# Kernel optimization log

Hardware: AMD Instinct MI355X
Metric: run time of the kernel (lower is better)

The kernel has to match this reference:

```python
import jax, jax.numpy as jnp
import numpy as np

N_NODES = 100000
FEAT = 256
HID = 128
REL = 2
BATCH = 20000
K = 10  # filtersize


def setup_inputs() -> dict:
    key = jax.random.key(0)
    k1, k2, k3, k4, k5 = jax.random.split(key, 5)
    nodes = jax.random.randint(k1, (BATCH,), 0, N_NODES)
    neigh_idx = jax.random.randint(k2, (REL, BATCH, K), 0, N_NODES)
    features = jax.random.normal(k3, (N_NODES, FEAT), dtype=jnp.float32)
    W_stc = jax.random.normal(k4, (REL, FEAT, HID), dtype=jnp.float32) * (1.0 / np.sqrt(FEAT))
    W_det = jax.random.normal(k5, (FEAT + REL * HID, HID), dtype=jnp.float32) * (1.0 / np.sqrt(FEAT + REL * HID))
    return {"nodes": nodes, "neigh_idx": neigh_idx, "features": features,
            "W_stc": W_stc, "W_det": W_det}


def reference(nodes, neigh_idx, features, W_stc, W_det):
    # self features: irregular gather [B, F]
    self_feats = features[nodes]
    # per-relation neighbor gather [R, B, K, F] -> mean over sampled neighbors [R, B, F]
    neigh_mean = features[neigh_idx].mean(axis=2)
    # STC layer projection to hidden per relation: [R, B, H]
    neigh_h = jnp.einsum('rbf,rfh->rbh', neigh_mean, W_stc)
    # concat self feats with each relation's neighbor embedding: [B, F + R*H]
    combined = jnp.concatenate(
        [self_feats, jnp.moveaxis(neigh_h, 0, 1).reshape(neigh_h.shape[1], -1)], axis=1)
    # linear + relu (dropout_flag=False -> no dropout)
    return jax.nn.relu(combined @ W_det)
```

## Files before the change

kernel.cpp:

```cpp
#include <hip/hip_runtime.h>
#include <hip/hip_bf16.h>

#define N_NODES 100000
#define FEAT    256
#define HID     128
#define REL     2
#define BATCH   20000
#define KNEI    10

#define APAD    8
#define AROW    (768 + APAD)

typedef short bf16x8 __attribute__((ext_vector_type(8)));
typedef float f32x4  __attribute__((ext_vector_type(4)));

__device__ __forceinline__ unsigned short f2bf(float x) {
    union { float f; unsigned u; } v; v.f = x;
    unsigned r = v.u + 0x7fffu + ((v.u >> 16) & 1u);
    return (unsigned short)(r >> 16);
}

__device__ __forceinline__ ushort4 pack4(float a, float b, float c, float d) {
    ushort4 p; p.x = f2bf(a); p.y = f2bf(b); p.z = f2bf(c); p.w = f2bf(d);
    return p;
}

__device__ __forceinline__ size_t bsw_index(int k, int n) {
    int kt = k >> 5, j = k & 7, hi = (k >> 3) & 3;
    int lane = hi * 16 + (n & 15), nt = n >> 4;
    return ((size_t)(kt * 8 + nt) * 64 + lane) * 8 + j;
}

__global__ __launch_bounds__(256) void prep_B(const float* __restrict__ W_stc,
                                              const float* __restrict__ W_det,
                                              unsigned short* __restrict__ Bsw) {
    const int blk = blockIdx.x;
    const int tid = threadIdx.x;
    if (blk < 256) {
        const int rel = blk >> 7;
        const int f   = (blk & 127) * 2 + (tid >> 7);
        const int n   = tid & 127;
        const float* ws = W_stc + (size_t)(rel * FEAT + f) * HID;
        const float* wd = W_det + (size_t)(256 + rel * HID) * HID + n;
        float acc = 0.f;
        #pragma unroll
        for (int j = 0; j < HID; ++j) acc += ws[j] * wd[(size_t)j * HID];
        Bsw[bsw_index(256 + rel * 256 + f, n)] = f2bf(acc);
    } else {
        const int base = (blk - 256) * 2048;
        #pragma unroll
        for (int i = 0; i < 8; ++i) {
            const int idx = base + i * 256 + tid;
            const int k = idx >> 7, n = idx & 127;
            Bsw[bsw_index(k, n)] = f2bf(W_det[idx]);
        }
    }
}

__global__ __launch_bounds__(256, 4) void fused(const int* __restrict__ nodes,
                                                const int* __restrict__ neigh_idx,
                                                const float* __restrict__ features,
                                                const unsigned short* __restrict__ Bsw,
                                                float* __restrict__ out) {
    __shared__ unsigned short As[16 * AROW];
    __shared__ int idxs[336];

    const int blk  = blockIdx.x;
    const int tid  = threadIdx.x;
    const int w    = tid >> 6;
    const int lane = tid & 63;
    const float inv = 1.0f / (float)KNEI;

    {
        if (tid < 16)       idxs[tid] = nodes[blk * 16 + tid];
        else if (tid < 176) idxs[tid] = neigh_idx[blk * 160 + (tid - 16)];
        else                idxs[tid] = neigh_idx[BATCH * KNEI + blk * 160 + (tid - 176)];
        const int t2 = tid + 256;
        if (t2 < 336)       idxs[t2] = neigh_idx[BATCH * KNEI + blk * 160 + (t2 - 176)];
    }
    __syncthreads();

    const unsigned lnoff = (unsigned)lane << 4;
    #pragma unroll
    for (int e = 0; e < 4; ++e) {
        const int m = w * 4 + e;

        int ia[11], ib[10];
        ia[0] = idxs[m];
        #pragma unroll
        for (int k = 0; k < KNEI; ++k) ia[1 + k] = idxs[16 + m * KNEI + k];
        #pragma unroll
        for (int k = 0; k < KNEI; ++k) ib[k]     = idxs[176 + m * KNEI + k];

        f32x4 ta[11];
        #pragma unroll
        for (int k = 0; k < 11; ++k) {
            const unsigned voff = ((unsigned)ia[k] << 10) + lnoff;
            asm volatile("global_load_dwordx4 %0, %1, %2"
                         : "=v"(ta[k]) : "v"(voff), "s"(features));
        }
        f32x4 tb[10];
        #pragma unroll
        for (int k = 0; k < KNEI; ++k) {
            const unsigned voff = ((unsigned)ib[k] << 10) + lnoff;
            asm volatile("global_load_dwordx4 %0, %1, %2"
                         : "=v"(tb[k]) : "v"(voff), "s"(features));
        }

        asm volatile("s_waitcnt vmcnt(10)" ::: "memory");
        __builtin_amdgcn_sched_barrier(0);

        f32x4 s0 = ta[1];
        #pragma unroll
        for (int k = 2; k < 11; ++k) s0 += ta[k];

        ushort4* row = (ushort4*)(As + m * AROW);
        row[lane]      = pack4(ta[0][0], ta[0][1], ta[0][2], ta[0][3]);
        row[64 + lane] = pack4(s0[0] * inv, s0[1] * inv, s0[2] * inv, s0[3] * inv);

        asm volatile("s_waitcnt vmcnt(0)" ::: "memory");
        __builtin_amdgcn_sched_barrier(0);

        f32x4 s1 = tb[0];
        #pragma unroll
        for (int k = 1; k < KNEI; ++k) s1 += tb[k];
        row[128 + lane] = pack4(s1[0] * inv, s1[1] * inv, s1[2] * inv, s1[3] * inv);
    }
    __syncthreads();

    const int quad = lane >> 4;
    const int l16  = lane & 15;
    const unsigned short* a_base = As + l16 * AROW + quad * 8;

    f32x4 acc0 = (f32x4){0.f, 0.f, 0.f, 0.f};
    f32x4 acc1 = (f32x4){0.f, 0.f, 0.f, 0.f};
    const int nt0 = w, nt1 = w + 4;

    #pragma unroll
    for (int kt = 0; kt < 24; ++kt) {
        bf16x8 a = *(const bf16x8*)(a_base + kt * 32);
        const unsigned short* bk = Bsw + ((size_t)(kt * 8) * 64 + lane) * 8;
        bf16x8 b0 = *(const bf16x8*)(bk + (size_t)nt0 * 64 * 8);
        bf16x8 b1 = *(const bf16x8*)(bk + (size_t)nt1 * 64 * 8);
        acc0 = __builtin_amdgcn_mfma_f32_16x16x32_bf16(a, b0, acc0, 0, 0, 0);
        acc1 = __builtin_amdgcn_mfma_f32_16x16x32_bf16(a, b1, acc1, 0, 0, 0);
    }

    float* orow = out + (size_t)(blk * 16) * HID;
    #pragma unroll
    for (int r = 0; r < 4; ++r) {
        const int row = quad * 4 + r;
        float v0 = acc0[r];
        float v1 = acc1[r];
        orow[(size_t)row * HID + nt0 * 16 + l16] = v0 > 0.f ? v0 : 0.f;
        orow[(size_t)row * HID + nt1 * 16 + l16] = v1 > 0.f ? v1 : 0.f;
    }
}

extern "C" void kernel_launch(void* const* d_in, const int* in_sizes, int n_in,
                              void* d_out, int out_size, void* d_ws, size_t ws_size,
                              hipStream_t stream) {
    const int*   nodes     = (const int*)d_in[0];
    const int*   neigh_idx = (const int*)d_in[1];
    const float* features  = (const float*)d_in[2];
    const float* W_stc     = (const float*)d_in[3];
    const float* W_det     = (const float*)d_in[4];
    float* out = (float*)d_out;

    unsigned short* Bsw = (unsigned short*)d_ws;

    prep_B<<<272, 256, 0, stream>>>(W_stc, W_det, Bsw);
    fused<<<BATCH / 16, 256, 0, stream>>>(nodes, neigh_idx, features, Bsw, out);
}
```

Baseline: 197.7 us.

## Pre-project all node features through W_stc, then gather projected rows

Adds a pass that multiplies every node's features by both relation W_stc matrices (fp16 MFMA) into a workspace table P. The fused kernel then averages gathered 128-wide fp16 rows of P instead of 256-wide fp32 feature rows, and its final GEMM shrinks from K=768 to K=512. Operands move from bf16 to fp16. The aim is to cut random-gather traffic, at the cost of a dense pass over all nodes (reading every feature row and writing P) and a large workspace requirement. The old path is kept as a fallback when the workspace is too small.

```diff
diff --git a/kernel.cpp b/kernel.cpp
--- a/kernel.cpp
+++ b/kernel.cpp
@@ -8,22 +8,194 @@
 #define BATCH   20000
 #define KNEI    10
 
-#define APAD    8
-#define AROW    (768 + APAD)
-
-typedef short bf16x8 __attribute__((ext_vector_type(8)));
-typedef float f32x4  __attribute__((ext_vector_type(4)));
+typedef short  bf16x8 __attribute__((ext_vector_type(8)));
+typedef _Float16 half8 __attribute__((ext_vector_type(8)));
+typedef float  f32x4  __attribute__((ext_vector_type(4)));
+
+__device__ __forceinline__ unsigned short f2h(float x) {
+    union { _Float16 h; unsigned short u; } t; t.h = (_Float16)x; return t.u;
+}
+__device__ __forceinline__ ushort4 pack4h(float a, float b, float c, float d) {
+    ushort4 p; p.x = f2h(a); p.y = f2h(b); p.z = f2h(c); p.w = f2h(d); return p;
+}
 
 __device__ __forceinline__ unsigned short f2bf(float x) {
     union { float f; unsigned u; } v; v.f = x;
     unsigned r = v.u + 0x7fffu + ((v.u >> 16) & 1u);
     return (unsigned short)(r >> 16);
 }
-
 __device__ __forceinline__ ushort4 pack4(float a, float b, float c, float d) {
-    ushort4 p; p.x = f2bf(a); p.y = f2bf(b); p.z = f2bf(c); p.w = f2bf(d);
-    return p;
-}
+    ushort4 p; p.x = f2bf(a); p.y = f2bf(b); p.z = f2bf(c); p.w = f2bf(d); return p;
+}
+
+__device__ __forceinline__ size_t bswi(int k, int n, int NT) {
+    int kt = k >> 5, j = k & 7, hi = (k >> 3) & 3;
+    int lane = hi * 16 + (n & 15), nt = n >> 4;
+    return ((size_t)(kt * NT + nt) * 64 + lane) * 8 + j;
+}
+
+
+__global__ __launch_bounds__(256) void prep_Bf16(const float* __restrict__ W_stc,
+                                                 const float* __restrict__ W_det,
+                                                 unsigned short* __restrict__ Bsw_det,
+                                                 unsigned short* __restrict__ Bsw_stc) {
+    const int blk = blockIdx.x, tid = threadIdx.x;
+    if (blk < 64) {
+        #pragma unroll
+        for (int i = 0; i < 4; ++i) {
+            const int idx = blk * 1024 + i * 256 + tid;
+            const int k = idx >> 7, n = idx & 127;
+            Bsw_det[bswi(k, n, 8)] = f2h(W_det[idx]);
+        }
+    } else {
+        #pragma unroll
+        for (int i = 0; i < 4; ++i) {
+            const int idx = (blk - 64) * 1024 + i * 256 + tid;
+            const int f = idx >> 8, n = idx & 255;
+            const int rel = n >> 7, h = n & 127;
+            Bsw_stc[bswi(f, n, 16)] = f2h(W_stc[(size_t)(rel * FEAT + f) * HID + h]);
+        }
+    }
+}
+
+#define APROW 264
+__global__ __launch_bounds__(256) void prep_P(const float* __restrict__ features,
+                                              const unsigned short* __restrict__ Bsw_stc,
+                                              unsigned short* __restrict__ P) {
+    __shared__ __align__(16) unsigned short Ap[16 * APROW];
+    __shared__ __align__(16) unsigned short Cs[16 * 256];
+    const int blk = blockIdx.x, tid = threadIdx.x;
+    const int w = tid >> 6, lane = tid & 63;
+    const float4* F4 = (const float4*)features;
+
+    #pragma unroll
+    for (int s = 0; s < 4; ++s) {
+        const int g = s * 256 + tid;
+        const int row = g >> 6, c4 = g & 63;
+        float4 v = F4[(size_t)(blk * 16 + row) * 64 + c4];
+        *(ushort4*)(Ap + row * APROW + c4 * 4) = pack4h(v.x, v.y, v.z, v.w);
+    }
+    __syncthreads();
+
+    const int quad = lane >> 4, l16 = lane & 15;
+    const unsigned short* a_base = Ap + l16 * APROW + quad * 8;
+    f32x4 acc[4] = {{0,0,0,0},{0,0,0,0},{0,0,0,0},{0,0,0,0}};
+    #pragma unroll
+    for (int kt = 0; kt < 8; ++kt) {
+        half8 a = *(const half8*)(a_base + kt * 32);
+        #pragma unroll
+        for (int t = 0; t < 4; ++t) {
+            const int nt = w + t * 4;
+            half8 b = *(const half8*)(Bsw_stc + ((size_t)(kt * 16 + nt) * 64 + lane) * 8);
+            acc[t] = __builtin_amdgcn_mfma_f32_16x16x32_f16(a, b, acc[t], 0, 0, 0);
+        }
+    }
+    #pragma unroll
+    for (int t = 0; t < 4; ++t) {
+        const int nt = w + t * 4;
+        #pragma unroll
+        for (int r = 0; r < 4; ++r)
+            Cs[(quad * 4 + r) * 256 + nt * 16 + l16] = f2h(acc[t][r]);
+    }
+    __syncthreads();
+
+    const int seg = tid >> 3, part = tid & 7;
+    const int row = seg >> 1, rel = seg & 1;
+    const unsigned short* src = Cs + row * 256 + rel * 128 + part * 16;
+    unsigned short* dst = P + (size_t)rel * N_NODES * HID
+                            + (size_t)(blk * 16 + row) * HID + part * 16;
+    *(uint4*)(dst)     = *(const uint4*)(src);
+    *(uint4*)(dst + 8) = *(const uint4*)(src + 8);
+}
+
+#define AROW2 520
+__global__ __launch_bounds__(256, 6) void fused2(const int* __restrict__ nodes,
+                                                 const int* __restrict__ neigh_idx,
+                                                 const float* __restrict__ features,
+                                                 const unsigned short* __restrict__ P,
+                                                 const unsigned short* __restrict__ Bsw_det,
+                                                 float* __restrict__ out) {
+    __shared__ __align__(16) unsigned short As[16 * AROW2];
+    __shared__ int idxs[336];
+
+    const int blk = blockIdx.x, tid = threadIdx.x;
+    const int w = tid >> 6, lane = tid & 63;
+    const int grp = lane >> 4, l16 = lane & 15;
+    const float4* F4 = (const float4*)features;
+    const float inv = 1.0f / (float)KNEI;
+
+    if (tid < 16)       idxs[tid] = nodes[blk * 16 + tid];
+    else if (tid < 176) idxs[tid] = neigh_idx[blk * 160 + (tid - 16)];
+    else                idxs[tid] = neigh_idx[BATCH * KNEI + blk * 160 + (tid - 176)];
+    const int t2 = tid + 256;
+    if (t2 < 336)       idxs[t2] = neigh_idx[BATCH * KNEI + blk * 160 + (t2 - 176)];
+    __syncthreads();
+
+    #pragma unroll
+    for (int e = 0; e < 4; ++e) {
+        const int m = w * 4 + e;
+        float4 sf = F4[(size_t)idxs[m] * 64 + lane];
+        *(ushort4*)(As + m * AROW2 + lane * 4) = pack4h(sf.x, sf.y, sf.z, sf.w);
+
+        #pragma unroll
+        for (int r = 0; r < 2; ++r) {
+            const int* ir = &idxs[16 + r * 160 + m * KNEI];
+            const unsigned short* Pr = P + (size_t)r * N_NODES * HID;
+            float acc[8] = {0.f,0.f,0.f,0.f,0.f,0.f,0.f,0.f};
+            #pragma unroll
+            for (int L = 0; L < 3; ++L) {
+                const int kk = L * 4 + grp;
+                const int nd = ir[kk < KNEI ? kk : KNEI - 1];
+                uint4 raw = *(const uint4*)(Pr + (size_t)nd * HID + l16 * 8);
+                float v[8];
+                union { unsigned u; _Float16 h[2]; } t;
+                t.u = raw.x; v[0] = (float)t.h[0]; v[1] = (float)t.h[1];
+                t.u = raw.y; v[2] = (float)t.h[0]; v[3] = (float)t.h[1];
+                t.u = raw.z; v[4] = (float)t.h[0]; v[5] = (float)t.h[1];
+                t.u = raw.w; v[6] = (float)t.h[0]; v[7] = (float)t.h[1];
+                if (L < 2 || lane < 32) {
+                    #pragma unroll
+                    for (int j = 0; j < 8; ++j) acc[j] += v[j];
+                }
+            }
+            #pragma unroll
+            for (int j = 0; j < 8; ++j) acc[j] += __shfl_xor(acc[j], 16);
+            #pragma unroll
+            for (int j = 0; j < 8; ++j) acc[j] += __shfl_xor(acc[j], 32);
+            if (lane < 16) {
+                unsigned short* d = As + m * AROW2 + 256 + r * 128 + lane * 8;
+                *(ushort4*)(d)     = pack4h(acc[0]*inv, acc[1]*inv, acc[2]*inv, acc[3]*inv);
+                *(ushort4*)(d + 4) = pack4h(acc[4]*inv, acc[5]*inv, acc[6]*inv, acc[7]*inv);
+            }
+        }
+    }
+    __syncthreads();
+
+    const unsigned short* a_base = As + l16 * AROW2 + grp * 8;
+    f32x4 acc0 = (f32x4){0.f,0.f,0.f,0.f};
+    f32x4 acc1 = (f32x4){0.f,0.f,0.f,0.f};
+    const int nt0 = w, nt1 = w + 4;
+    #pragma unroll
+    for (int kt = 0; kt < 16; ++kt) {
+        half8 a = *(const half8*)(a_base + kt * 32);
+        const unsigned short* bk = Bsw_det + ((size_t)(kt * 8) * 64 + lane) * 8;
+        half8 b0 = *(const half8*)(bk + (size_t)nt0 * 512);
+        half8 b1 = *(const half8*)(bk + (size_t)nt1 * 512);
+        acc0 = __builtin_amdgcn_mfma_f32_16x16x32_f16(a, b0, acc0, 0, 0, 0);
+        acc1 = __builtin_amdgcn_mfma_f32_16x16x32_f16(a, b1, acc1, 0, 0, 0);
+    }
+    float* orow = out + (size_t)(blk * 16) * HID;
+    #pragma unroll
+    for (int r = 0; r < 4; ++r) {
+        const int row = grp * 4 + r;
+        float v0 = acc0[r], v1 = acc1[r];
+        orow[(size_t)row * HID + nt0 * 16 + l16] = v0 > 0.f ? v0 : 0.f;
+        orow[(size_t)row * HID + nt1 * 16 + l16] = v1 > 0.f ? v1 : 0.f;
+    }
+}
+
+#define APAD    8
+#define AROW    (768 + APAD)
 
 __device__ __forceinline__ size_t bsw_index(int k, int n) {
     int kt = k >> 5, j = k & 7, hi = (k >> 3) & 3;
@@ -31,9 +203,9 @@
     return ((size_t)(kt * 8 + nt) * 64 + lane) * 8 + j;
 }
 
-__global__ __launch_bounds__(256) void prep_B(const float* __restrict__ W_stc,
-                                              const float* __restrict__ W_det,
-                                              unsigned short* __restrict__ Bsw) {
+__global__ __launch_bounds__(256) void prep_B_old(const float* __restrict__ W_stc,
+                                                  const float* __restrict__ W_det,
+                                                  unsigned short* __restrict__ Bsw) {
     const int blk = blockIdx.x;
     const int tid = threadIdx.x;
     if (blk < 256) {
@@ -57,11 +229,11 @@
     }
 }
 
-__global__ __launch_bounds__(256, 4) void fused(const int* __restrict__ nodes,
-                                                const int* __restrict__ neigh_idx,
-                                                const float* __restrict__ features,
-                                                const unsigned short* __restrict__ Bsw,
-                                                float* __restrict__ out) {
+__global__ __launch_bounds__(256, 4) void fused_old(const int* __restrict__ nodes,
+                                                    const int* __restrict__ neigh_idx,
+                                                    const float* __restrict__ features,
+                                                    const unsigned short* __restrict__ Bsw,
+                                                    float* __restrict__ out) {
     __shared__ unsigned short As[16 * AROW];
     __shared__ int idxs[336];
 
@@ -71,20 +243,17 @@
     const int lane = tid & 63;
     const float inv = 1.0f / (float)KNEI;
 
-    {
-        if (tid < 16)       idxs[tid] = nodes[blk * 16 + tid];
-        else if (tid < 176) idxs[tid] = neigh_idx[blk * 160 + (tid - 16)];
-        else                idxs[tid] = neigh_idx[BATCH * KNEI + blk * 160 + (tid - 176)];
-        const int t2 = tid + 256;
-        if (t2 < 336)       idxs[t2] = neigh_idx[BATCH * KNEI + blk * 160 + (t2 - 176)];
-    }
+    if (tid < 16)       idxs[tid] = nodes[blk * 16 + tid];
+    else if (tid < 176) idxs[tid] = neigh_idx[blk * 160 + (tid - 16)];
+    else                idxs[tid] = neigh_idx[BATCH * KNEI + blk * 160 + (tid - 176)];
+    const int t2 = tid + 256;
+    if (t2 < 336)       idxs[t2] = neigh_idx[BATCH * KNEI + blk * 160 + (t2 - 176)];
     __syncthreads();
 
     const unsigned lnoff = (unsigned)lane << 4;
     #pragma unroll
     for (int e = 0; e < 4; ++e) {
         const int m = w * 4 + e;
-
         int ia[11], ib[10];
         ia[0] = idxs[m];
         #pragma unroll
@@ -167,8 +336,21 @@
     const float* W_det     = (const float*)d_in[4];
     float* out = (float*)d_out;
 
-    unsigned short* Bsw = (unsigned short*)d_ws;
-
-    prep_B<<<272, 256, 0, stream>>>(W_stc, W_det, Bsw);
-    fused<<<BATCH / 16, 256, 0, stream>>>(nodes, neigh_idx, features, Bsw, out);
-}
+    const size_t P_BYTES   = (size_t)REL * N_NODES * HID * 2;
+    const size_t BD_BYTES  = 512 * 128 * 2;
+    const size_t BS_BYTES  = 256 * 256 * 2;
+    const size_t WS_NEEDED = P_BYTES + BD_BYTES + BS_BYTES;
+
+    if (ws_size >= WS_NEEDED) {
+        unsigned short* P       = (unsigned short*)d_ws;
+        unsigned short* Bsw_det = (unsigned short*)((char*)d_ws + P_BYTES);
+        unsigned short* Bsw_stc = (unsigned short*)((char*)d_ws + P_BYTES + BD_BYTES);
+        prep_Bf16<<<128, 256, 0, stream>>>(W_stc, W_det, Bsw_det, Bsw_stc);
+        prep_P<<<N_NODES / 16, 256, 0, stream>>>(features, Bsw_stc, P);
+        fused2<<<BATCH / 16, 256, 0, stream>>>(nodes, neigh_idx, features, P, Bsw_det, out);
+    } else {
+        unsigned short* Bsw = (unsigned short*)d_ws;
+        prep_B_old<<<272, 256, 0, stream>>>(W_stc, W_det, Bsw);
+        fused_old<<<BATCH / 16, 256, 0, stream>>>(nodes, neigh_idx, features, Bsw, out);
+    }
+}
```

Result: slower. 210.5 us (+6.5%).

## Convert feature table to fp16 before gathering to halve gather bytes

Applied to the files above, without the earlier changes.

Adds a pre-pass that converts the full fp32 feature table to fp16 in workspace. The fused kernel then gathers 8-byte fp16 chunks per lane instead of 16-byte fp32 chunks and accumulates in fp32. The aim is to cut the bytes moved by the random row gathers. In exchange, every call pays for a full-table conversion pass and some precision is lost. The old fp32 path is kept as a fallback when the workspace is too small.

```diff
diff --git a/kernel.cpp b/kernel.cpp
--- a/kernel.cpp
+++ b/kernel.cpp
@@ -11,24 +11,47 @@
 #define APAD    8
 #define AROW    (768 + APAD)
 
-typedef short bf16x8 __attribute__((ext_vector_type(8)));
-typedef float f32x4  __attribute__((ext_vector_type(4)));
+typedef short  bf16x8 __attribute__((ext_vector_type(8)));
+typedef float  f32x4  __attribute__((ext_vector_type(4)));
+typedef unsigned u32x2 __attribute__((ext_vector_type(2)));
 
 __device__ __forceinline__ unsigned short f2bf(float x) {
     union { float f; unsigned u; } v; v.f = x;
     unsigned r = v.u + 0x7fffu + ((v.u >> 16) & 1u);
     return (unsigned short)(r >> 16);
 }
-
 __device__ __forceinline__ ushort4 pack4(float a, float b, float c, float d) {
     ushort4 p; p.x = f2bf(a); p.y = f2bf(b); p.z = f2bf(c); p.w = f2bf(d);
     return p;
+}
+__device__ __forceinline__ unsigned short f2h(float x) {
+    union { _Float16 h; unsigned short u; } t; t.h = (_Float16)x; return t.u;
+}
+__device__ __forceinline__ ushort4 pack4h(float a, float b, float c, float d) {
+    ushort4 p; p.x = f2h(a); p.y = f2h(b); p.z = f2h(c); p.w = f2h(d); return p;
+}
+__device__ __forceinline__ void h4acc(u32x2 r, float4& s) {
+    union { unsigned u; _Float16 h[2]; } t;
+    t.u = r.x; s.x += (float)t.h[0]; s.y += (float)t.h[1];
+    t.u = r.y; s.z += (float)t.h[0]; s.w += (float)t.h[1];
 }
 
 __device__ __forceinline__ size_t bsw_index(int k, int n) {
     int kt = k >> 5, j = k & 7, hi = (k >> 3) & 3;
     int lane = hi * 16 + (n & 15), nt = n >> 4;
     return ((size_t)(kt * 8 + nt) * 64 + lane) * 8 + j;
+}
+
+__global__ __launch_bounds__(256) void conv_h(const float* __restrict__ features,
+                                              unsigned short* __restrict__ Fh) {
+    const int stride = gridDim.x * blockDim.x;
+    const int n4 = N_NODES * FEAT / 4;
+    const float4* src = (const float4*)features;
+    ushort4* dst = (ushort4*)Fh;
+    for (int i = blockIdx.x * blockDim.x + threadIdx.x; i < n4; i += stride) {
+        float4 v = src[i];
+        dst[i] = pack4h(v.x, v.y, v.z, v.w);
+    }
 }
 
 __global__ __launch_bounds__(256) void prep_B(const float* __restrict__ W_stc,
@@ -57,11 +80,11 @@
     }
 }
 
-__global__ __launch_bounds__(256, 4) void fused(const int* __restrict__ nodes,
-                                                const int* __restrict__ neigh_idx,
-                                                const float* __restrict__ features,
-                                                const unsigned short* __restrict__ Bsw,
-                                                float* __restrict__ out) {
+__global__ __launch_bounds__(256, 4) void fused_h(const int* __restrict__ nodes,
+                                                  const int* __restrict__ neigh_idx,
+                                                  const unsigned short* __restrict__ Fh,
+                                                  const unsigned short* __restrict__ Bsw,
+                                                  float* __restrict__ out) {
     __shared__ unsigned short As[16 * AROW];
     __shared__ int idxs[336];
 
@@ -71,20 +94,116 @@
     const int lane = tid & 63;
     const float inv = 1.0f / (float)KNEI;
 
-    {
-        if (tid < 16)       idxs[tid] = nodes[blk * 16 + tid];
-        else if (tid < 176) idxs[tid] = neigh_idx[blk * 160 + (tid - 16)];
-        else                idxs[tid] = neigh_idx[BATCH * KNEI + blk * 160 + (tid - 176)];
-        const int t2 = tid + 256;
-        if (t2 < 336)       idxs[t2] = neigh_idx[BATCH * KNEI + blk * 160 + (t2 - 176)];
-    }
+    if (tid < 16)       idxs[tid] = nodes[blk * 16 + tid];
+    else if (tid < 176) idxs[tid] = neigh_idx[blk * 160 + (tid - 16)];
+    else                idxs[tid] = neigh_idx[BATCH * KNEI + blk * 160 + (tid - 176)];
+    const int t2 = tid + 256;
+    if (t2 < 336)       idxs[t2] = neigh_idx[BATCH * KNEI + blk * 160 + (t2 - 176)];
     __syncthreads();
 
-    const unsigned lnoff = (unsigned)lane << 4;
+    const unsigned lnoff = (unsigned)lane << 3;
     #pragma unroll
     for (int e = 0; e < 4; ++e) {
         const int m = w * 4 + e;
-
+        int ia[11], ib[10];
+        ia[0] = idxs[m];
+        #pragma unroll
+        for (int k = 0; k < KNEI; ++k) ia[1 + k] = idxs[16 + m * KNEI + k];
+        #pragma unroll
+        for (int k = 0; k < KNEI; ++k) ib[k]     = idxs[176 + m * KNEI + k];
+
+        u32x2 ta[11];
+        #pragma unroll
+        for (int k = 0; k < 11; ++k) {
+            const unsigned voff = ((unsigned)ia[k] << 9) + lnoff;
+            asm volatile("global_load_dwordx2 %0, %1, %2"
+                         : "=v"(ta[k]) : "v"(voff), "s"(Fh));
+        }
+        u32x2 tb[10];
+        #pragma unroll
+        for (int k = 0; k < KNEI; ++k) {
+            const unsigned voff = ((unsigned)ib[k] << 9) + lnoff;
+            asm volatile("global_load_dwordx2 %0, %1, %2"
+                         : "=v"(tb[k]) : "v"(voff), "s"(Fh));
+        }
+
+        asm volatile("s_waitcnt vmcnt(10)" ::: "memory");
+        __builtin_amdgcn_sched_barrier(0);
+
+        float4 sf = make_float4(0.f, 0.f, 0.f, 0.f);
+        h4acc(ta[0], sf);
+        float4 s0 = make_float4(0.f, 0.f, 0.f, 0.f);
+        #pragma unroll
+        for (int k = 1; k < 11; ++k) h4acc(ta[k], s0);
+
+        ushort4* row = (ushort4*)(As + m * AROW);
+        row[lane]      = pack4(sf.x, sf.y, sf.z, sf.w);
+        row[64 + lane] = pack4(s0.x * inv, s0.y * inv, s0.z * inv, s0.w * inv);
+
+        asm volatile("s_waitcnt vmcnt(0)" ::: "memory");
+        __builtin_amdgcn_sched_barrier(0);
+
+        float4 s1 = make_float4(0.f, 0.f, 0.f, 0.f);
+        #pragma unroll
+        for (int k = 0; k < KNEI; ++k) h4acc(tb[k], s1);
+        row[128 + lane] = pack4(s1.x * inv, s1.y * inv, s1.z * inv, s1.w * inv);
+    }
+    __syncthreads();
+
+    const int quad = lane >> 4;
+    const int l16  = lane & 15;
+    const unsigned short* a_base = As + l16 * AROW + quad * 8;
+
+    f32x4 acc0 = (f32x4){0.f, 0.f, 0.f, 0.f};
+    f32x4 acc1 = (f32x4){0.f, 0.f, 0.f, 0.f};
+    const int nt0 = w, nt1 = w + 4;
+
+    #pragma unroll
+    for (int kt = 0; kt < 24; ++kt) {
+        bf16x8 a = *(const bf16x8*)(a_base + kt * 32);
+        const unsigned short* bk = Bsw + ((size_t)(kt * 8) * 64 + lane) * 8;
+        bf16x8 b0 = *(const bf16x8*)(bk + (size_t)nt0 * 64 * 8);
+        bf16x8 b1 = *(const bf16x8*)(bk + (size_t)nt1 * 64 * 8);
+        acc0 = __builtin_amdgcn_mfma_f32_16x16x32_bf16(a, b0, acc0, 0, 0, 0);
+        acc1 = __builtin_amdgcn_mfma_f32_16x16x32_bf16(a, b1, acc1, 0, 0, 0);
+    }
+
+    float* orow = out + (size_t)(blk * 16) * HID;
+    #pragma unroll
+    for (int r = 0; r < 4; ++r) {
+        const int row = quad * 4 + r;
+        float v0 = acc0[r];
+        float v1 = acc1[r];
+        orow[(size_t)row * HID + nt0 * 16 + l16] = v0 > 0.f ? v0 : 0.f;
+        orow[(size_t)row * HID + nt1 * 16 + l16] = v1 > 0.f ? v1 : 0.f;
+    }
+}
+
+__global__ __launch_bounds__(256, 4) void fused_old(const int* __restrict__ nodes,
+                                                    const int* __restrict__ neigh_idx,
+                                                    const float* __restrict__ features,
+                                                    const unsigned short* __restrict__ Bsw,
+                                                    float* __restrict__ out) {
+    __shared__ unsigned short As[16 * AROW];
+    __shared__ int idxs[336];
+
+    const int blk  = blockIdx.x;
+    const int tid  = threadIdx.x;
+    const int w    = tid >> 6;
+    const int lane = tid & 63;
+    const float inv = 1.0f / (float)KNEI;
+
+    if (tid < 16)       idxs[tid] = nodes[blk * 16 + tid];
+    else if (tid < 176) idxs[tid] = neigh_idx[blk * 160 + (tid - 16)];
+    else                idxs[tid] = neigh_idx[BATCH * KNEI + blk * 160 + (tid - 176)];
+    const int t2 = tid + 256;
+    if (t2 < 336)       idxs[t2] = neigh_idx[BATCH * KNEI + blk * 160 + (t2 - 176)];
+    __syncthreads();
+
+    const unsigned lnoff = (unsigned)lane << 4;
+    #pragma unroll
+    for (int e = 0; e < 4; ++e) {
+        const int m = w * 4 + e;
         int ia[11], ib[10];
         ia[0] = idxs[m];
         #pragma unroll
@@ -167,8 +286,19 @@
     const float* W_det     = (const float*)d_in[4];
     float* out = (float*)d_out;
 
-    unsigned short* Bsw = (unsigned short*)d_ws;
-
-    prep_B<<<272, 256, 0, stream>>>(W_stc, W_det, Bsw);
-    fused<<<BATCH / 16, 256, 0, stream>>>(nodes, neigh_idx, features, Bsw, out);
-}
+    const size_t FH_BYTES  = (size_t)N_NODES * FEAT * 2;
+    const size_t BSW_BYTES = 768 * 128 * 2;
+    const size_t WS_NEEDED = FH_BYTES + BSW_BYTES;
+
+    if (ws_size >= WS_NEEDED) {
+        unsigned short* Fh  = (unsigned short*)d_ws;
+        unsigned short* Bsw = (unsigned short*)((char*)d_ws + FH_BYTES);
+        conv_h<<<2048, 256, 0, stream>>>(features, Fh);
+        prep_B<<<272, 256, 0, stream>>>(W_stc, W_det, Bsw);
+        fused_h<<<BATCH / 16, 256, 0, stream>>>(nodes, neigh_idx, Fh, Bsw, out);
+    } else {
+        unsigned short* Bsw = (unsigned short*)d_ws;
+        prep_B<<<272, 256, 0, stream>>>(W_stc, W_det, Bsw);
+        fused_old<<<BATCH / 16, 256, 0, stream>>>(nodes, neigh_idx, features, Bsw, out);
+    }
+}
```

Result: slower. 204.3 us (+3.3%).
